# Kernel tuning notes

Hardware: AMD Instinct MI355X
Metric: run time of the kernel (lower is better)

Reference implementation:

```python
import jax, jax.numpy as jnp
import numpy as np

N = 8192      # points
K = 16        # nsample neighbors
CIN = 64      # in_plane
C = 256       # out_plane (== mid_planes)
S = 8         # share_planes
EPS = 1e-5


def _bn(x, g, b, axes):
    # BatchNorm1d (training-mode batch stats, biased var), channel = last dim
    m = x.mean(axes, keepdims=True)
    v = x.var(axes, keepdims=True)
    return (x - m) / jnp.sqrt(v + EPS) * g + b


def _knn(p, k):
    # brute-force KNN over a single batch (o = [N]); indices include self
    sq = jnp.sum(p * p, axis=1)
    d2 = sq[:, None] + sq[None, :] - 2.0 * (p @ p.T)   # [N, N]
    idx = jax.lax.top_k(-d2, k)[1]                      # [N, K]
    return jax.lax.stop_gradient(idx)


def setup_inputs() -> dict:
    key = jax.random.key(0)
    ks = jax.random.split(key, 16)
    W = lambda i, shp, s=0.05: jax.random.normal(ks[i], shp, jnp.float32) * s
    one = lambda d: jnp.ones((d,), jnp.float32)
    zero = lambda d: jnp.zeros((d,), jnp.float32)
    return {
        "p": jax.random.normal(ks[0], (N, 3), jnp.float32),
        "x": jax.random.normal(ks[1], (N, CIN), jnp.float32),
        "o": jnp.array([N], dtype=jnp.int32),
        # PointAggregation (stride=1): Linear(no bias) + BN
        "W_pa": W(2, (CIN, C)), "g_pa": one(C), "b_pa": zero(C),
        # SelfFusion.linear1 (no bias) + bn1
        "W1": W(3, (C, C)), "g1": one(C), "b1": zero(C),
        # SelfFusionLayer q/k/v
        "Wq": W(4, (C, C)), "bq": zero(C),
        "Wk": W(5, (C, C)), "bk": zero(C),
        "Wv": W(6, (C, C)), "bv": zero(C),
        # linear_p: Linear(3,3)+BN(3)+ReLU+Linear(3,C)
        "Wp1": W(7, (3, 3), 0.3), "bp1": zero(3), "gp": one(3), "bp": zero(3),
        "Wp2": W(8, (3, C), 0.3), "bp2": zero(C),
        # linear_w: BN(C)+ReLU+Linear(C,C//S)+BN(C//S)+ReLU+Linear(C//S,C//S)
        "gw1": one(C), "bw1": zero(C),
        "Ww1": W(9, (C, C // S)), "bww1": zero(C // S),
        "gw2": one(C // S), "bw2": zero(C // S),
        "Ww2": W(10, (C // S, C // S), 0.2), "bww2": zero(C // S),
        # bn2, linear3 (no bias) + bn3
        "g2": one(C), "b2": zero(C),
        "W3": W(11, (C, C)), "g3": one(C), "b3": zero(C),
    }


def reference(p, x, o, W_pa, g_pa, b_pa, W1, g1, b1, Wq, bq, Wk, bk, Wv, bv,
              Wp1, bp1, gp, bp, Wp2, bp2, gw1, bw1, Ww1, bww1, gw2, bw2,
              Ww2, bww2, g2, b2, W3, g3, b3):
    relu = jax.nn.relu
    # --- PointAggregation (stride=1) ---
    h = relu(_bn(x @ W_pa, g_pa, b_pa, (0,)))          # [N, C]
    # --- SelfFusion block ---
    identity = h
    h = relu(_bn(h @ W1, g1, b1, (0,)))                # [N, C]
    # SelfFusionLayer
    xq = h @ Wq + bq                                   # [N, C]
    xk = h @ Wk + bk
    xv = h @ Wv + bv
    idx = _knn(p, K)                                   # [N, K]
    rel = p[idx] - p[:, None, :]                       # [N, K, 3] relative coords
    xk_g = xk[idx]                                     # [N, K, C]
    xv_g = xv[idx]                                     # [N, K, C]
    # linear_p: Linear(3,3) -> BN(3) -> ReLU -> Linear(3,C)
    p_r = rel @ Wp1 + bp1
    p_r = relu(_bn(p_r, gp, bp, (0, 1)))
    p_r = p_r @ Wp2 + bp2                              # [N, K, C]
    # mid_planes == out_planes so view(...).sum(2) is identity
    w = xk_g - xq[:, None, :] + p_r                    # [N, K, C]
    # linear_w: BN -> ReLU -> Linear -> BN -> ReLU -> Linear
    w = relu(_bn(w, gw1, bw1, (0, 1)))
    w = w @ Ww1 + bww1                                 # [N, K, C//S]
    w = relu(_bn(w, gw2, bw2, (0, 1)))
    w = w @ Ww2 + bww2                                 # [N, K, C//S]
    w = jax.nn.softmax(w, axis=1)                      # softmax over neighbors
    y = ((xv_g + p_r).reshape(N, K, S, C // S) * w[:, :, None, :]).sum(1)
    y = y.reshape(N, C)
    # back in SelfFusion
    y = relu(_bn(y, g2, b2, (0,)))
    y = _bn(y @ W3, g3, b3, (0,))
    x2 = relu(y + identity)
    return (p, x2, o)
```

## Files before the change

kernel.cpp:

```cpp
#include <hip/hip_runtime.h>
#include <hip/hip_bf16.h>

#define INV_N  (1.0f/8192.0f)
#define INV_NK (1.0f/131072.0f)

typedef __attribute__((ext_vector_type(8))) short bf16x8;
typedef __attribute__((ext_vector_type(4))) float f32x4;
typedef unsigned short u16;

__device__ __forceinline__ u16 f2b(float f) {
  unsigned u = __float_as_uint(f);
  return (u16)((u + 0x7FFFu + ((u >> 16) & 1u)) >> 16);
}
__device__ __forceinline__ float b2f(u16 u) {
  return __uint_as_float(((unsigned)u) << 16);
}

__device__ __forceinline__ float bn_ap(float v, const float* st, int C, int ch,
                                       float inv, float g, float b) {
  float m = st[ch] * inv;
  float var = st[C + ch] * inv - m * m;
  return (v - m) * rsqrtf(var + 1e-5f) * g + b;
}

__launch_bounds__(256)
__global__ void prep_k(const float* __restrict__ p, const int* __restrict__ o,
                       const float* __restrict__ Ww1,
                       float4* __restrict__ pp, u16* __restrict__ Ww1t,
                       float* __restrict__ out) {
  int b = blockIdx.x, t = threadIdx.x;
  int e = b*256 + t;
  if (e < 24576) out[e] = p[e];
  if (e == 0) out[24576 + 2097152] = (float)o[0];
  if (e < 8192) {
    float x = p[e*3+0], y = p[e*3+1], z = p[e*3+2];
    pp[e] = make_float4(x, y, z, (x*x + y*y) + z*z);
  }
  if (b >= 88) {
    int q = (b - 88)*1024 + t*4;
#pragma unroll
    for (int ii = 0; ii < 4; ++ii) {
      int e2 = q + ii;
      int k = e2 >> 5, n = e2 & 31;
      Ww1t[n*256 + k] = f2b(Ww1[e2]);
    }
  }
}

template<int ROWS, int SPLIT>
__launch_bounds__(256)
__global__ void red_k(const float* __restrict__ part, float* __restrict__ outp,
                      int width) {
  int ncg = width >> 6;
  int cg = blockIdx.x % ncg, sp = blockIdx.x / ncg;
  int lane = threadIdx.x & 63, chunk = threadIdx.x >> 6;
  int c = cg*64 + lane;
  constexpr int R  = ROWS / SPLIT;
  constexpr int RC = R / 4;
  float s = 0.f;
  int i0 = sp*R + chunk*RC;
#pragma unroll 4
  for (int i = i0; i < i0 + RC; ++i) s += part[(size_t)i*width + c];
  __shared__ float red[4][64];
  red[chunk][lane] = s;
  __syncthreads();
  if (threadIdx.x < 64) {
    float v = red[0][lane] + red[1][lane] + red[2][lane] + red[3][lane];
    if (SPLIT == 1) outp[c] = v;
    else atomicAdd(&outp[c], v);
  }
}

__launch_bounds__(256)
__global__ void knn_k(const float4* __restrict__ pp, int* __restrict__ idxo) {
  int wave = threadIdx.x >> 6;
  int lane = threadIdx.x & 63;
  int q = blockIdx.x*4 + wave;
  float4 qv = pp[q];
  const float BIG = __uint_as_float(0x7F7FFFFFu);
  float d[4];
#pragma unroll
  for (int s = 0; s < 4; ++s) d[s] = BIG;
#pragma unroll 4
  for (int it = 0; it < 128; ++it) {
    int j = it*64 + lane;
    float4 c = pp[j];
    float dot = qv.x*c.x + (qv.y*c.y + qv.z*c.z);
    float d2 = __fmaf_rn(-2.0f, dot, qv.w + c.w);
    float pk = __uint_as_float((__float_as_uint(d2) & 0xFFFFE000u) | (unsigned)j);
#pragma unroll
    for (int s = 3; s >= 1; --s)
      d[s] = fminf(fmaxf(d[s-1], pk), d[s]);
    d[0] = fminf(d[0], pk);
  }
  for (int r = 0; r < 16; ++r) {
    float bd = d[0];
#pragma unroll
    for (int m = 1; m < 64; m <<= 1)
      bd = fminf(bd, __shfl_xor(bd, m));
    if (lane == 0) idxo[q*16 + r] = (int)(__float_as_uint(bd) & 0x1FFFu);
    if (d[0] == bd) {
#pragma unroll
      for (int s = 0; s < 3; ++s) d[s] = d[s+1];
      d[3] = BIG;
    }
  }
}

template<bool BNA, bool STATS>
__launch_bounds__(256)
__global__ void mfgemm_k(const float* __restrict__ A, const float* __restrict__ st,
                         const float* __restrict__ g, const float* __restrict__ bb,
                         float inv_cnt,
                         const float* __restrict__ W, float* __restrict__ out,
                         float* __restrict__ stout, int KA, int NOUT) {
  __shared__ short As[64][72];
  __shared__ short Bt[64][72];
  __shared__ float lscl[256], lsft[256];
  int t = threadIdx.x;
  int m0 = blockIdx.x * 64, n0 = blockIdx.y * 64;
  if (BNA) {
    for (int e = t; e < KA; e += 256) {
      float m = st[e] * inv_cnt;
      float var = st[KA + e] * inv_cnt - m*m;
      float sc = rsqrtf(var + 1e-5f) * g[e];
      lscl[e] = sc; lsft[e] = bb[e] - m*sc;
    }
    __syncthreads();
  }
  const f32x4 zero = {0.f, 0.f, 0.f, 0.f};
  f32x4 acc[2][2] = {{zero, zero}, {zero, zero}};
  int wv = t >> 6, l = t & 63;
  int wm = wv & 1, wn = wv >> 1;
  int lr = l & 15, lk = (l >> 4) * 8;
  int ra = t >> 4, qa = t & 15;
  int bn = t & 63, bkc = t >> 6;
  for (int k0 = 0; k0 < KA; k0 += 64) {
#pragma unroll
    for (int rp = 0; rp < 4; ++rp) {
      int r = rp*16 + ra;
      float4 av = *(const float4*)(A + (size_t)(m0 + r)*KA + k0 + qa*4);
      float vv[4] = {av.x, av.y, av.z, av.w};
      short4 s;
#pragma unroll
      for (int jj = 0; jj < 4; ++jj) {
        float v = vv[jj];
        if (BNA) { int ch = k0 + qa*4 + jj; v = fmaxf(fmaf(v, lscl[ch], lsft[ch]), 0.f); }
        ((u16*)&s)[jj] = f2b(v);
      }
      *(short4*)&As[r][qa*4] = s;
    }
    {
      float v[16];
#pragma unroll
      for (int j2 = 0; j2 < 16; ++j2)
        v[j2] = W[(size_t)(k0 + bkc*16 + j2)*NOUT + n0 + bn];
      bf16x8 w0, w1v;
#pragma unroll
      for (int j2 = 0; j2 < 8; ++j2) {
        w0[j2]  = (short)f2b(v[j2]);
        w1v[j2] = (short)f2b(v[8 + j2]);
      }
      *(bf16x8*)&Bt[bn][bkc*16]     = w0;
      *(bf16x8*)&Bt[bn][bkc*16 + 8] = w1v;
    }
    __syncthreads();
#pragma unroll
    for (int fk = 0; fk < 2; ++fk) {
      bf16x8 a0 = *(const bf16x8*)&As[wm*32 +      lr][fk*32 + lk];
      bf16x8 a1 = *(const bf16x8*)&As[wm*32 + 16 + lr][fk*32 + lk];
      bf16x8 b0 = *(const bf16x8*)&Bt[wn*32 +      lr][fk*32 + lk];
      bf16x8 b1 = *(const bf16x8*)&Bt[wn*32 + 16 + lr][fk*32 + lk];
      acc[0][0] = __builtin_amdgcn_mfma_f32_16x16x32_bf16(a0, b0, acc[0][0], 0, 0, 0);
      acc[0][1] = __builtin_amdgcn_mfma_f32_16x16x32_bf16(a0, b1, acc[0][1], 0, 0, 0);
      acc[1][0] = __builtin_amdgcn_mfma_f32_16x16x32_bf16(a1, b0, acc[1][0], 0, 0, 0);
      acc[1][1] = __builtin_amdgcn_mfma_f32_16x16x32_bf16(a1, b1, acc[1][1], 0, 0, 0);
    }
    __syncthreads();
  }
#pragma unroll
  for (int fn = 0; fn < 2; ++fn) {
    int col = n0 + wn*32 + fn*16 + lr;
    float s1 = 0.f, s2 = 0.f;
#pragma unroll
    for (int fm = 0; fm < 2; ++fm) {
#pragma unroll
      for (int r = 0; r < 4; ++r) {
        int row = m0 + wm*32 + fm*16 + (l >> 4)*4 + r;
        float v = acc[fm][fn][r];
        out[(size_t)row*NOUT + col] = v;
        if (STATS) { s1 += v; s2 += v*v; }
      }
    }
    if (STATS) {
      s1 += __shfl_xor(s1, 16); s1 += __shfl_xor(s1, 32);
      s2 += __shfl_xor(s2, 16); s2 += __shfl_xor(s2, 32);
      if (l < 16) {
        atomicAdd(&stout[col], s1);
        atomicAdd(&stout[NOUT + col], s2);
      }
    }
  }
}

__launch_bounds__(256)
__global__ void qkv_k(const float* __restrict__ t1, const float* __restrict__ st,
                      const float* __restrict__ g1, const float* __restrict__ b1,
                      const float* __restrict__ Wq, const float* __restrict__ bq,
                      const float* __restrict__ Wk, const float* __restrict__ bk,
                      const float* __restrict__ Wv, const float* __restrict__ bv,
                      u16* __restrict__ xq, u16* __restrict__ xk, u16* __restrict__ xv) {
  __shared__ short As[64][72];
  __shared__ short Bt[3][64][72];
  __shared__ float lscl[256], lsft[256];
  int t = threadIdx.x;
  int m0 = blockIdx.x * 64, n0 = blockIdx.y * 64;
  {
    int e = t;
    float m = st[e] * INV_N;
    float var = st[256 + e] * INV_N - m*m;
    float sc = rsqrtf(var + 1e-5f) * g1[e];
    lscl[e] = sc; lsft[e] = b1[e] - m*sc;
  }
  __syncthreads();
  const f32x4 zero = {0.f, 0.f, 0.f, 0.f};
  f32x4 acc[3][2][2];
#pragma unroll
  for (int w = 0; w < 3; ++w)
#pragma unroll
    for (int i = 0; i < 2; ++i)
#pragma unroll
      for (int j = 0; j < 2; ++j) acc[w][i][j] = zero;
  int wv = t >> 6, l = t & 63;
  int wm = wv & 1, wn = wv >> 1;
  int lr = l & 15, lk = (l >> 4) * 8;
  int ra = t >> 4, qa = t & 15;
  int bn = t & 63, bkc = t >> 6;
  const float* Ws[3] = {Wq, Wk, Wv};
  for (int k0 = 0; k0 < 256; k0 += 64) {
#pragma unroll
    for (int rp = 0; rp < 4; ++rp) {
      int r = rp*16 + ra;
      float4 av = *(const float4*)(t1 + (size_t)(m0 + r)*256 + k0 + qa*4);
      float vv[4] = {av.x, av.y, av.z, av.w};
      short4 s;
#pragma unroll
      for (int jj = 0; jj < 4; ++jj) {
        int ch = k0 + qa*4 + jj;
        float v = fmaxf(fmaf(vv[jj], lscl[ch], lsft[ch]), 0.f);
        ((u16*)&s)[jj] = f2b(v);
      }
      *(short4*)&As[r][qa*4] = s;
    }
#pragma unroll
    for (int w = 0; w < 3; ++w) {
      float v[16];
#pragma unroll
      for (int j2 = 0; j2 < 16; ++j2)
        v[j2] = Ws[w][(size_t)(k0 + bkc*16 + j2)*256 + n0 + bn];
      bf16x8 w0, w1v;
#pragma unroll
      for (int j2 = 0; j2 < 8; ++j2) {
        w0[j2]  = (short)f2b(v[j2]);
        w1v[j2] = (short)f2b(v[8 + j2]);
      }
      *(bf16x8*)&Bt[w][bn][bkc*16]     = w0;
      *(bf16x8*)&Bt[w][bn][bkc*16 + 8] = w1v;
    }
    __syncthreads();
#pragma unroll
    for (int fk = 0; fk < 2; ++fk) {
      bf16x8 a0 = *(const bf16x8*)&As[wm*32 +      lr][fk*32 + lk];
      bf16x8 a1 = *(const bf16x8*)&As[wm*32 + 16 + lr][fk*32 + lk];
#pragma unroll
      for (int w = 0; w < 3; ++w) {
        bf16x8 b0 = *(const bf16x8*)&Bt[w][wn*32 +      lr][fk*32 + lk];
        bf16x8 b1 = *(const bf16x8*)&Bt[w][wn*32 + 16 + lr][fk*32 + lk];
        acc[w][0][0] = __builtin_amdgcn_mfma_f32_16x16x32_bf16(a0, b0, acc[w][0][0], 0, 0, 0);
        acc[w][0][1] = __builtin_amdgcn_mfma_f32_16x16x32_bf16(a0, b1, acc[w][0][1], 0, 0, 0);
        acc[w][1][0] = __builtin_amdgcn_mfma_f32_16x16x32_bf16(a1, b0, acc[w][1][0], 0, 0, 0);
        acc[w][1][1] = __builtin_amdgcn_mfma_f32_16x16x32_bf16(a1, b1, acc[w][1][1], 0, 0, 0);
      }
    }
    __syncthreads();
  }
  u16* outs[3] = {xq, xk, xv};
  const float* bs[3] = {bq, bk, bv};
#pragma unroll
  for (int w = 0; w < 3; ++w) {
#pragma unroll
    for (int fn = 0; fn < 2; ++fn) {
      int col = n0 + wn*32 + fn*16 + lr;
      float bvv = bs[w][col];
#pragma unroll
      for (int fm = 0; fm < 2; ++fm) {
#pragma unroll
        for (int r = 0; r < 4; ++r) {
          int row = m0 + wm*32 + fm*16 + (l >> 4)*4 + r;
          outs[w][(size_t)row*256 + col] = f2b(acc[w][fm][fn][r] + bvv);
        }
      }
    }
  }
}

__launch_bounds__(256)
__global__ void stats256_k(const float* __restrict__ X, float* __restrict__ psy) {
  int c = threadIdx.x;
  int r0 = blockIdx.x * 32;
  float s1 = 0.f, s2 = 0.f;
  for (int r = 0; r < 32; ++r) {
    float v = X[(size_t)(r0 + r)*256 + c];
    s1 += v; s2 += v*v;
  }
  psy[(size_t)blockIdx.x*512 + c]       = s1;
  psy[(size_t)blockIdx.x*512 + 256 + c] = s2;
}

__device__ __forceinline__ void comp_pr1(const float* p, int i, int j,
                                         const float* Wp1, const float* bp1,
                                         float pr1[3]) {
  float rx = p[j*3+0] - p[i*3+0];
  float ry = p[j*3+1] - p[i*3+1];
  float rz = p[j*3+2] - p[i*3+2];
#pragma unroll
  for (int c = 0; c < 3; ++c)
    pr1[c] = rx*Wp1[c] + ry*Wp1[3+c] + rz*Wp1[6+c] + bp1[c];
}

__device__ __forceinline__ void comp_prv(const float* p, int i, int j,
                                         const float* Wp1, const float* bp1,
                                         const float* gp, const float* bpp,
                                         const float* sp, float o3[3]) {
  float pr1[3];
  comp_pr1(p, i, j, Wp1, bp1, pr1);
#pragma unroll
  for (int c = 0; c < 3; ++c)
    o3[c] = fmaxf(bn_ap(pr1[c], sp, 3, c, INV_NK, gp[c], bpp[c]), 0.0f);
}

__launch_bounds__(256)
__global__ void prstats_k(const float* __restrict__ p, const int* __restrict__ idx,
                          const float* Wp1, const float* bp1, float* __restrict__ sp) {
  float s[3] = {0,0,0}, s2[3] = {0,0,0};
  for (int it = 0; it < 4; ++it) {
    int e = blockIdx.x*1024 + it*256 + threadIdx.x;
    int i = e >> 4;
    int j = idx[e] & 8191;
    float pr1[3];
    comp_pr1(p, i, j, Wp1, bp1, pr1);
#pragma unroll
    for (int c = 0; c < 3; ++c) { s[c] += pr1[c]; s2[c] += pr1[c]*pr1[c]; }
  }
#pragma unroll
  for (int m = 1; m < 64; m <<= 1) {
#pragma unroll
    for (int c = 0; c < 3; ++c) {
      s[c]  += __shfl_xor(s[c],  m);
      s2[c] += __shfl_xor(s2[c], m);
    }
  }
  __shared__ float red[4][6];
  int wv = threadIdx.x >> 6, lane = threadIdx.x & 63;
  if (lane == 0) {
#pragma unroll
    for (int c = 0; c < 3; ++c) { red[wv][c] = s[c]; red[wv][3+c] = s2[c]; }
  }
  __syncthreads();
  if (threadIdx.x < 6) {
    float v = red[0][threadIdx.x] + red[1][threadIdx.x] +
              red[2][threadIdx.x] + red[3][threadIdx.x];
    atomicAdd(&sp[threadIdx.x], v);
  }
}

__launch_bounds__(256)
__global__ void wstats_k(const u16* __restrict__ xk, const u16* __restrict__ xq,
                         const float* __restrict__ p, const int* __restrict__ idx,
                         const float* Wp1, const float* bp1, const float* gp, const float* bpp,
                         const float* sp, const float* __restrict__ Wp2, const float* bp2,
                         float* __restrict__ pws) {
  __shared__ float prv[8][16][4];
  __shared__ int   jidx[8][16];
  int base = blockIdx.x * 8;
  int t = threadIdx.x;
  if (t < 128) {
    int pt = t >> 4, k = t & 15;
    int j = idx[(base + pt)*16 + k] & 8191;
    jidx[pt][k] = j;
    float o3[3];
    comp_prv(p, base + pt, j, Wp1, bp1, gp, bpp, sp, o3);
    prv[pt][k][0] = o3[0]; prv[pt][k][1] = o3[1]; prv[pt][k][2] = o3[2];
  }
  __syncthreads();
  int c = t;
  float wp0 = Wp2[c], wp1v = Wp2[256+c], wp2v = Wp2[512+c];
  float bbv = bp2[c];
  float s1 = 0.f, s2 = 0.f;
  for (int pt = 0; pt < 8; ++pt) {
    int i = base + pt;
    float xqv = b2f(xq[(size_t)i*256 + c]);
    u16 kvals[16];
#pragma unroll
    for (int k = 0; k < 16; ++k)
      kvals[k] = xk[(size_t)jidx[pt][k]*256 + c];
#pragma unroll
    for (int k = 0; k < 16; ++k) {
      float pr = prv[pt][k][0]*wp0 + prv[pt][k][1]*wp1v + prv[pt][k][2]*wp2v + bbv;
      float wval = b2f(kvals[k]) - xqv + pr;
      s1 += wval; s2 += wval*wval;
    }
  }
  pws[(size_t)blockIdx.x*512 + c]       = s1;
  pws[(size_t)blockIdx.x*512 + 256 + c] = s2;
}

__launch_bounds__(256)
__global__ void w1gemm_k(const u16* __restrict__ xk, const u16* __restrict__ xq,
                         const float* __restrict__ p, const int* __restrict__ idx,
                         const float* Wp1, const float* bp1, const float* gp, const float* bpp,
                         const float* sp, const float* __restrict__ Wp2, const float* bp2,
                         const float* sw, const float* gw1, const float* bw1,
                         const u16* __restrict__ Ww1t, const float* bww1,
                         u16* __restrict__ w1, float* __restrict__ pw1) {
  __shared__ short sA[64][264];
  __shared__ float prv[64][3];
  __shared__ int   jrow[64];
  __shared__ float sred[256];
  int t = threadIdx.x;
  int base4 = blockIdx.x * 4;
  if (t < 64) {
    int grow = blockIdx.x*64 + t;
    int j = idx[grow] & 8191;
    jrow[t] = j;
    float o3[3];
    comp_prv(p, grow >> 4, j, Wp1, bp1, gp, bpp, sp, o3);
    prv[t][0] = o3[0]; prv[t][1] = o3[1]; prv[t][2] = o3[2];
  }
  __syncthreads();
  {
    int o = t & 31, rs = t >> 5;
    int ch0 = o*8;
    int jr[8];
#pragma unroll
    for (int ii = 0; ii < 8; ++ii) jr[ii] = jrow[ii*8 + rs];
    bf16x8 kvv[8], qvv[8];
#pragma unroll
    for (int ii = 0; ii < 8; ++ii) {
      int r = ii*8 + rs;
      kvv[ii] = *(const bf16x8*)(xk + (size_t)jr[ii]*256 + ch0);
      qvv[ii] = *(const bf16x8*)(xq + (size_t)(base4 + (r >> 4))*256 + ch0);
    }
    float sclv[8], sftv[8], w0v[8], w1vv[8], w2v[8], b2v[8];
#pragma unroll
    for (int h = 0; h < 2; ++h) {
      float4 swm = *(const float4*)(sw + ch0 + h*4);
      float4 sws = *(const float4*)(sw + 256 + ch0 + h*4);
      float4 g4  = *(const float4*)(gw1 + ch0 + h*4);
      float4 bb4 = *(const float4*)(bw1 + ch0 + h*4);
      float4 p0v = *(const float4*)(Wp2 + ch0 + h*4);
      float4 p1v = *(const float4*)(Wp2 + 256 + ch0 + h*4);
      float4 p2v = *(const float4*)(Wp2 + 512 + ch0 + h*4);
      float4 bp4 = *(const float4*)(bp2 + ch0 + h*4);
      float mv[4] = {swm.x, swm.y, swm.z, swm.w};
      float sv[4] = {sws.x, sws.y, sws.z, sws.w};
      float gv[4] = {g4.x, g4.y, g4.z, g4.w};
      float bv[4] = {bb4.x, bb4.y, bb4.z, bb4.w};
      float a0[4] = {p0v.x, p0v.y, p0v.z, p0v.w};
      float a1[4] = {p1v.x, p1v.y, p1v.z, p1v.w};
      float a2[4] = {p2v.x, p2v.y, p2v.z, p2v.w};
      float a3[4] = {bp4.x, bp4.y, bp4.z, bp4.w};
#pragma unroll
      for (int jj = 0; jj < 4; ++jj) {
        int e = h*4 + jj;
        float m = mv[jj]*INV_NK;
        float var = sv[jj]*INV_NK - m*m;
        float sc = rsqrtf(var + 1e-5f)*gv[jj];
        sclv[e] = sc; sftv[e] = bv[jj] - m*sc;
        w0v[e] = a0[jj]; w1vv[e] = a1[jj]; w2v[e] = a2[jj]; b2v[e] = a3[jj];
      }
    }
#pragma unroll
    for (int ii = 0; ii < 8; ++ii) {
      int r = ii*8 + rs;
      float p0 = prv[r][0], p1 = prv[r][1], p2 = prv[r][2];
      bf16x8 av;
#pragma unroll
      for (int e = 0; e < 8; ++e) {
        float v = b2f((u16)kvv[ii][e]) - b2f((u16)qvv[ii][e])
                + p0*w0v[e] + p1*w1vv[e] + p2*w2v[e] + b2v[e];
        v = fmaxf(fmaf(v, sclv[e], sftv[e]), 0.f);
        av[e] = (short)f2b(v);
      }
      *(bf16x8*)&sA[r][ch0] = av;
    }
  }
  __syncthreads();
  const f32x4 zero = {0.f,0.f,0.f,0.f};
  f32x4 acc[2] = {zero, zero};
  int wv = t >> 6, l = t & 63;
  int lr = l & 15, hi = l >> 4;
#pragma unroll
  for (int k0 = 0; k0 < 8; ++k0) {
    int kb = k0*32 + hi*8;
    bf16x8 a  = *(const bf16x8*)&sA[wv*16 + lr][kb];
    bf16x8 b0 = *(const bf16x8*)(Ww1t + (size_t)lr*256      + kb);
    bf16x8 b1 = *(const bf16x8*)(Ww1t + (size_t)(16+lr)*256 + kb);
    acc[0] = __builtin_amdgcn_mfma_f32_16x16x32_bf16(a, b0, acc[0], 0, 0, 0);
    acc[1] = __builtin_amdgcn_mfma_f32_16x16x32_bf16(a, b1, acc[1], 0, 0, 0);
  }
#pragma unroll
  for (int fn = 0; fn < 2; ++fn) {
    int col = fn*16 + lr;
    float bv = bww1[col];
    float s1 = 0.f, s2 = 0.f;
#pragma unroll
    for (int r = 0; r < 4; ++r) {
      int grow = blockIdx.x*64 + wv*16 + hi*4 + r;
      float v = acc[fn][r] + bv;
      w1[(size_t)grow*32 + col] = f2b(v);
      s1 += v; s2 += v*v;
    }
    s1 += __shfl_xor(s1, 16); s1 += __shfl_xor(s1, 32);
    s2 += __shfl_xor(s2, 16); s2 += __shfl_xor(s2, 32);
    if (l < 16) { sred[(wv*2+fn)*16 + lr] = s1; sred[128 + (wv*2+fn)*16 + lr] = s2; }
  }
  __syncthreads();
  if (t < 32) {
    float a = 0.f, b = 0.f;
#pragma unroll
    for (int w2 = 0; w2 < 4; ++w2) {
      a += sred[(w2*2 + (t >> 4))*16 + (t & 15)];
      b += sred[128 + (w2*2 + (t >> 4))*16 + (t & 15)];
    }
    pw1[(size_t)blockIdx.x*64 + t]      = a;
    pw1[(size_t)blockIdx.x*64 + 32 + t] = b;
  }
}

__launch_bounds__(256)
__global__ void aggr_k(const u16* __restrict__ w1, const float* sw1,
                       const float* gw2, const float* bw2,
                       const float* __restrict__ Ww2, const float* bww2,
                       const u16* __restrict__ xv,
                       const float* __restrict__ p, const int* __restrict__ idx,
                       const float* Wp1, const float* bp1, const float* gp, const float* bpp,
                       const float* sp, const float* __restrict__ Wp2, const float* bp2,
                       float* __restrict__ y) {
  __shared__ float lw1[16][32];
  __shared__ float lW2[32][32];
  __shared__ float sw2[16][33];
  __shared__ float prv[16][4];
  __shared__ int   jidx[16];
  int i = blockIdx.x, t = threadIdx.x;
  for (int e = t; e < 1024; e += 256) lW2[e >> 5][e & 31] = Ww2[e];
  for (int e = t; e < 512; e += 256) {
    int c32 = e & 31;
    float v = b2f(w1[(size_t)i*512 + e]);
    v = fmaxf(bn_ap(v, sw1, 32, c32, INV_NK, gw2[c32], bw2[c32]), 0.0f);
    lw1[e >> 5][c32] = v;
  }
  if (t < 16) jidx[t] = idx[i*16 + t] & 8191;
  __syncthreads();
  if (t < 16) {
    float o3[3];
    comp_prv(p, i, jidx[t], Wp1, bp1, gp, bpp, sp, o3);
    prv[t][0] = o3[0]; prv[t][1] = o3[1]; prv[t][2] = o3[2];
  }
  for (int e = t; e < 512; e += 256) {
    int k = e >> 5, c32 = e & 31;
    float a = bww2[c32];
#pragma unroll
    for (int j = 0; j < 32; ++j) a += lw1[k][j] * lW2[j][c32];
    sw2[k][c32] = a;
  }
  __syncthreads();
  if (t < 32) {
    float mx = -3.0e38f;
#pragma unroll
    for (int k = 0; k < 16; ++k) mx = fmaxf(mx, sw2[k][t]);
    float s = 0.f;
#pragma unroll
    for (int k = 0; k < 16; ++k) { float e2 = expf(sw2[k][t] - mx); sw2[k][t] = e2; s += e2; }
    float r = 1.0f / s;
#pragma unroll
    for (int k = 0; k < 16; ++k) sw2[k][t] *= r;
  }
  __syncthreads();
  int c = t;
  float wp0 = Wp2[c], wp1v = Wp2[256+c], wp2v = Wp2[512+c];
  float bbv = bp2[c];
  int c32 = c & 31;
  float acc = 0.f;
#pragma unroll
  for (int k = 0; k < 16; ++k) {
    int j = jidx[k];
    float pr = prv[k][0]*wp0 + prv[k][1]*wp1v + prv[k][2]*wp2v + bbv;
    float xvv = b2f(xv[(size_t)j*256 + c]);
    acc += (xvv + pr) * sw2[k][c32];
  }
  y[(size_t)i*256 + c] = acc;
}

__launch_bounds__(256)
__global__ void final_k(const float* __restrict__ t0, const float* s0,
                        const float* g0, const float* b0,
                        const float* __restrict__ t3, const float* s3,
                        const float* g3, const float* b3,
                        float* __restrict__ out) {
  int i = blockIdx.x, c = threadIdx.x;
  size_t off = (size_t)i*256 + c;
  float h0 = fmaxf(bn_ap(t0[off], s0, 256, c, INV_N, g0[c], b0[c]), 0.0f);
  float v3 = bn_ap(t3[off], s3, 256, c, INV_N, g3[c], b3[c]);
  out[24576 + off] = fmaxf(v3 + h0, 0.0f);
}

extern "C" void kernel_launch(void* const* d_in, const int* in_sizes, int n_in,
                              void* d_out, int out_size, void* d_ws, size_t ws_size,
                              hipStream_t stream) {
  (void)in_sizes; (void)n_in; (void)out_size; (void)ws_size;
  const float* p    = (const float*)d_in[0];
  const float* x    = (const float*)d_in[1];
  const int*   o    = (const int*)  d_in[2];
  const float* W_pa = (const float*)d_in[3];
  const float* g_pa = (const float*)d_in[4];
  const float* b_pa = (const float*)d_in[5];
  const float* W1   = (const float*)d_in[6];
  const float* g1   = (const float*)d_in[7];
  const float* b1   = (const float*)d_in[8];
  const float* Wq   = (const float*)d_in[9];
  const float* bq   = (const float*)d_in[10];
  const float* Wk   = (const float*)d_in[11];
  const float* bk   = (const float*)d_in[12];
  const float* Wv   = (const float*)d_in[13];
  const float* bv   = (const float*)d_in[14];
  const float* Wp1  = (const float*)d_in[15];
  const float* bp1  = (const float*)d_in[16];
  const float* gp   = (const float*)d_in[17];
  const float* bpp  = (const float*)d_in[18];
  const float* Wp2  = (const float*)d_in[19];
  const float* bp2  = (const float*)d_in[20];
  const float* gw1  = (const float*)d_in[21];
  const float* bw1  = (const float*)d_in[22];
  const float* Ww1  = (const float*)d_in[23];
  const float* bww1 = (const float*)d_in[24];
  const float* gw2  = (const float*)d_in[25];
  const float* bw2  = (const float*)d_in[26];
  const float* Ww2  = (const float*)d_in[27];
  const float* bww2 = (const float*)d_in[28];
  const float* g2   = (const float*)d_in[29];
  const float* b2   = (const float*)d_in[30];
  const float* W3   = (const float*)d_in[31];
  const float* g3   = (const float*)d_in[32];
  const float* b3   = (const float*)d_in[33];

  char* ws = (char*)d_ws;
  float* t0  = (float*)(ws + 0);
  float* t1  = (float*)(ws + 8388608);
  u16*   xq  = (u16*)  (ws + 16777216);
  u16*   xk  = (u16*)  (ws + 20971520);
  u16*   xv  = (u16*)  (ws + 25165824);
  u16*   w1  = (u16*)  (ws + 29360128);
  int*   idx = (int*)  (ws + 37748736);
  float* st  = (float*)(ws + 38273024);
  u16*   Ww1t= (u16*)  (ws + 38289408);
  float* pw1 = (float*)(ws + 41943040);
  float* pws = (float*)(ws + 42467328);
  float* psy = (float*)(ws + 44564480);
  float* y   = t1;
  float* t3  = (float*)(ws + 16777216);
  float4* pp = (float4*)(ws + 29360128);

  hipMemsetAsync(st, 0, 16384, stream);

  prep_k<<<96, 256, 0, stream>>>(p, o, Ww1, pp, Ww1t, (float*)d_out);
  knn_k<<<2048, 256, 0, stream>>>(pp, idx);

  mfgemm_k<false, true><<<dim3(128, 4), 256, 0, stream>>>(
      x, nullptr, nullptr, nullptr, 0.f, W_pa, t0, st + 0, 64, 256);

  mfgemm_k<true, true><<<dim3(128, 4), 256, 0, stream>>>(
      t0, st + 0, g_pa, b_pa, INV_N, W1, t1, st + 512, 256, 256);

  qkv_k<<<dim3(128, 4), 256, 0, stream>>>(
      t1, st + 512, g1, b1, Wq, bq, Wk, bk, Wv, bv, xq, xk, xv);

  prstats_k<<<128, 256, 0, stream>>>(p, idx, Wp1, bp1, st + 2624);

  wstats_k<<<1024, 256, 0, stream>>>(xk, xq, p, idx, Wp1, bp1, gp, bpp,
                                     st + 2624, Wp2, bp2, pws);
  red_k<1024, 4><<<32, 256, 0, stream>>>(pws, st + 1024, 512);

  w1gemm_k<<<2048, 256, 0, stream>>>(xk, xq, p, idx, Wp1, bp1, gp, bpp,
                                     st + 2624, Wp2, bp2, st + 1024,
                                     gw1, bw1, Ww1t, bww1, w1, pw1);
  red_k<2048, 16><<<16, 256, 0, stream>>>(pw1, st + 2560, 64);

  aggr_k<<<8192, 256, 0, stream>>>(w1, st + 2560, gw2, bw2, Ww2, bww2, xv,
                                   p, idx, Wp1, bp1, gp, bpp, st + 2624,
                                   Wp2, bp2, y);
  stats256_k<<<256, 256, 0, stream>>>(y, psy);
  red_k<256, 2><<<16, 256, 0, stream>>>(psy, st + 1536, 512);

  mfgemm_k<true, true><<<dim3(128, 4), 256, 0, stream>>>(
      y, st + 1536, g2, b2, INV_N, W3, t3, st + 2048, 256, 256);

  final_k<<<8192, 256, 0, stream>>>(t0, st + 0, g_pa, b_pa,
                                    t3, st + 2048, g3, b3, (float*)d_out);
}
```

Baseline: 210.7 us.

## Store intermediate activations in bf16 and shrink KNN per-lane candidate list

```diff
diff --git a/kernel.cpp b/kernel.cpp
--- a/kernel.cpp
+++ b/kernel.cpp
@@ -78,9 +78,9 @@
   int q = blockIdx.x*4 + wave;
   float4 qv = pp[q];
   const float BIG = __uint_as_float(0x7F7FFFFFu);
-  float d[4];
-#pragma unroll
-  for (int s = 0; s < 4; ++s) d[s] = BIG;
+  float d[3];
+#pragma unroll
+  for (int s = 0; s < 3; ++s) d[s] = BIG;
 #pragma unroll 4
   for (int it = 0; it < 128; ++it) {
     int j = it*64 + lane;
@@ -88,9 +88,8 @@
     float dot = qv.x*c.x + (qv.y*c.y + qv.z*c.z);
     float d2 = __fmaf_rn(-2.0f, dot, qv.w + c.w);
     float pk = __uint_as_float((__float_as_uint(d2) & 0xFFFFE000u) | (unsigned)j);
-#pragma unroll
-    for (int s = 3; s >= 1; --s)
-      d[s] = fminf(fmaxf(d[s-1], pk), d[s]);
+    d[2] = fminf(fmaxf(d[1], pk), d[2]);
+    d[1] = fminf(fmaxf(d[0], pk), d[1]);
     d[0] = fminf(d[0], pk);
   }
   for (int r = 0; r < 16; ++r) {
@@ -100,19 +99,17 @@
       bd = fminf(bd, __shfl_xor(bd, m));
     if (lane == 0) idxo[q*16 + r] = (int)(__float_as_uint(bd) & 0x1FFFu);
     if (d[0] == bd) {
-#pragma unroll
-      for (int s = 0; s < 3; ++s) d[s] = d[s+1];
-      d[3] = BIG;
-    }
-  }
-}
-
-template<bool BNA, bool STATS>
-__launch_bounds__(256)
-__global__ void mfgemm_k(const float* __restrict__ A, const float* __restrict__ st,
+      d[0] = d[1]; d[1] = d[2]; d[2] = BIG;
+    }
+  }
+}
+
+template<typename TA, typename TO, bool BNA, bool STATS>
+__launch_bounds__(256)
+__global__ void mfgemm_k(const TA* __restrict__ A, const float* __restrict__ st,
                          const float* __restrict__ g, const float* __restrict__ bb,
                          float inv_cnt,
-                         const float* __restrict__ W, float* __restrict__ out,
+                         const float* __restrict__ W, TO* __restrict__ out,
                          float* __restrict__ stout, int KA, int NOUT) {
   __shared__ short As[64][72];
   __shared__ short Bt[64][72];
@@ -139,8 +136,15 @@
 #pragma unroll
     for (int rp = 0; rp < 4; ++rp) {
       int r = rp*16 + ra;
-      float4 av = *(const float4*)(A + (size_t)(m0 + r)*KA + k0 + qa*4);
-      float vv[4] = {av.x, av.y, av.z, av.w};
+      float vv[4];
+      if constexpr (sizeof(TA) == 4) {
+        float4 av = *(const float4*)((const float*)A + (size_t)(m0 + r)*KA + k0 + qa*4);
+        vv[0] = av.x; vv[1] = av.y; vv[2] = av.z; vv[3] = av.w;
+      } else {
+        short4 av = *(const short4*)((const u16*)A + (size_t)(m0 + r)*KA + k0 + qa*4);
+#pragma unroll
+        for (int jj = 0; jj < 4; ++jj) vv[jj] = b2f(((u16*)&av)[jj]);
+      }
       short4 s;
 #pragma unroll
       for (int jj = 0; jj < 4; ++jj) {
@@ -188,7 +192,8 @@
       for (int r = 0; r < 4; ++r) {
         int row = m0 + wm*32 + fm*16 + (l >> 4)*4 + r;
         float v = acc[fm][fn][r];
-        out[(size_t)row*NOUT + col] = v;
+        if constexpr (sizeof(TO) == 4) out[(size_t)row*NOUT + col] = v;
+        else                           out[(size_t)row*NOUT + col] = f2b(v);
         if (STATS) { s1 += v; s2 += v*v; }
       }
     }
@@ -204,7 +209,7 @@
 }
 
 __launch_bounds__(256)
-__global__ void qkv_k(const float* __restrict__ t1, const float* __restrict__ st,
+__global__ void qkv_k(const u16* __restrict__ t1, const float* __restrict__ st,
                       const float* __restrict__ g1, const float* __restrict__ b1,
                       const float* __restrict__ Wq, const float* __restrict__ bq,
                       const float* __restrict__ Wk, const float* __restrict__ bk,
@@ -241,13 +246,12 @@
 #pragma unroll
     for (int rp = 0; rp < 4; ++rp) {
       int r = rp*16 + ra;
-      float4 av = *(const float4*)(t1 + (size_t)(m0 + r)*256 + k0 + qa*4);
-      float vv[4] = {av.x, av.y, av.z, av.w};
+      short4 av = *(const short4*)(t1 + (size_t)(m0 + r)*256 + k0 + qa*4);
       short4 s;
 #pragma unroll
       for (int jj = 0; jj < 4; ++jj) {
         int ch = k0 + qa*4 + jj;
-        float v = fmaxf(fmaf(vv[jj], lscl[ch], lsft[ch]), 0.f);
+        float v = fmaxf(fmaf(b2f(((u16*)&av)[jj]), lscl[ch], lsft[ch]), 0.f);
         ((u16*)&s)[jj] = f2b(v);
       }
       *(short4*)&As[r][qa*4] = s;
@@ -305,12 +309,12 @@
 }
 
 __launch_bounds__(256)
-__global__ void stats256_k(const float* __restrict__ X, float* __restrict__ psy) {
+__global__ void stats256_k(const u16* __restrict__ X, float* __restrict__ psy) {
   int c = threadIdx.x;
   int r0 = blockIdx.x * 32;
   float s1 = 0.f, s2 = 0.f;
   for (int r = 0; r < 32; ++r) {
-    float v = X[(size_t)(r0 + r)*256 + c];
+    float v = b2f(X[(size_t)(r0 + r)*256 + c]);
     s1 += v; s2 += v*v;
   }
   psy[(size_t)blockIdx.x*512 + c]       = s1;
@@ -546,7 +550,7 @@
                        const float* __restrict__ p, const int* __restrict__ idx,
                        const float* Wp1, const float* bp1, const float* gp, const float* bpp,
                        const float* sp, const float* __restrict__ Wp2, const float* bp2,
-                       float* __restrict__ y) {
+                       u16* __restrict__ y) {
   __shared__ float lw1[16][32];
   __shared__ float lW2[32][32];
   __shared__ float sw2[16][33];
@@ -599,19 +603,19 @@
     float xvv = b2f(xv[(size_t)j*256 + c]);
     acc += (xvv + pr) * sw2[k][c32];
   }
-  y[(size_t)i*256 + c] = acc;
-}
-
-__launch_bounds__(256)
-__global__ void final_k(const float* __restrict__ t0, const float* s0,
+  y[(size_t)i*256 + c] = f2b(acc);
+}
+
+__launch_bounds__(256)
+__global__ void final_k(const u16* __restrict__ t0, const float* s0,
                         const float* g0, const float* b0,
-                        const float* __restrict__ t3, const float* s3,
+                        const u16* __restrict__ t3, const float* s3,
                         const float* g3, const float* b3,
                         float* __restrict__ out) {
   int i = blockIdx.x, c = threadIdx.x;
   size_t off = (size_t)i*256 + c;
-  float h0 = fmaxf(bn_ap(t0[off], s0, 256, c, INV_N, g0[c], b0[c]), 0.0f);
-  float v3 = bn_ap(t3[off], s3, 256, c, INV_N, g3[c], b3[c]);
+  float h0 = fmaxf(bn_ap(b2f(t0[off]), s0, 256, c, INV_N, g0[c], b0[c]), 0.0f);
+  float v3 = bn_ap(b2f(t3[off]), s3, 256, c, INV_N, g3[c], b3[c]);
   out[24576 + off] = fmaxf(v3 + h0, 0.0f);
 }
 
@@ -655,31 +659,31 @@
   const float* b3   = (const float*)d_in[33];
 
   char* ws = (char*)d_ws;
-  float* t0  = (float*)(ws + 0);
-  float* t1  = (float*)(ws + 8388608);
-  u16*   xq  = (u16*)  (ws + 16777216);
-  u16*   xk  = (u16*)  (ws + 20971520);
-  u16*   xv  = (u16*)  (ws + 25165824);
-  u16*   w1  = (u16*)  (ws + 29360128);
-  int*   idx = (int*)  (ws + 37748736);
-  float* st  = (float*)(ws + 38273024);
-  u16*   Ww1t= (u16*)  (ws + 38289408);
-  float* pw1 = (float*)(ws + 41943040);
-  float* pws = (float*)(ws + 42467328);
-  float* psy = (float*)(ws + 44564480);
-  float* y   = t1;
-  float* t3  = (float*)(ws + 16777216);
-  float4* pp = (float4*)(ws + 29360128);
+  u16*   t0  = (u16*)  (ws + 0);
+  u16*   t1  = (u16*)  (ws + 4194304);
+  u16*   xq  = (u16*)  (ws + 8388608);
+  u16*   xk  = (u16*)  (ws + 12582912);
+  u16*   xv  = (u16*)  (ws + 16777216);
+  u16*   w1  = (u16*)  (ws + 20971520);
+  int*   idx = (int*)  (ws + 29360128);
+  float* st  = (float*)(ws + 29884416);
+  u16*   Ww1t= (u16*)  (ws + 29900800);
+  float* pw1 = (float*)(ws + 30408704);
+  float* pws = (float*)(ws + 30932992);
+  float* psy = (float*)(ws + 33030144);
+  u16*   y   = t1;
+  u16*   t3  = xq;
+  float4* pp = (float4*)(ws + 20971520);
 
   hipMemsetAsync(st, 0, 16384, stream);
 
   prep_k<<<96, 256, 0, stream>>>(p, o, Ww1, pp, Ww1t, (float*)d_out);
   knn_k<<<2048, 256, 0, stream>>>(pp, idx);
 
-  mfgemm_k<false, true><<<dim3(128, 4), 256, 0, stream>>>(
+  mfgemm_k<float, u16, false, true><<<dim3(128, 4), 256, 0, stream>>>(
       x, nullptr, nullptr, nullptr, 0.f, W_pa, t0, st + 0, 64, 256);
 
-  mfgemm_k<true, true><<<dim3(128, 4), 256, 0, stream>>>(
+  mfgemm_k<u16, u16, true, true><<<dim3(128, 4), 256, 0, stream>>>(
       t0, st + 0, g_pa, b_pa, INV_N, W1, t1, st + 512, 256, 256);
 
   qkv_k<<<dim3(128, 4), 256, 0, stream>>>(
@@ -702,7 +706,7 @@
   stats256_k<<<256, 256, 0, stream>>>(y, psy);
   red_k<256, 2><<<16, 256, 0, stream>>>(psy, st + 1536, 512);
 
-  mfgemm_k<true, true><<<dim3(128, 4), 256, 0, stream>>>(
+  mfgemm_k<u16, u16, true, true><<<dim3(128, 4), 256, 0, stream>>>(
       y, st + 1536, g2, b2, INV_N, W3, t3, st + 2048, 256, 256);
 
   final_k<<<8192, 256, 0, stream>>>(t0, st + 0, g_pa, b_pa,
```

Result: faster. 205.6 us (-2.4%).
